# Kernel tuning notes

Measured on AMD Instinct MI355X. Metric: run time of the kernel, lower is better.

## Reference

```python
import jax, jax.numpy as jnp
import numpy as np

NUM_EXPERT = 8
TOP_K = 1


def setup_inputs() -> dict:
    key = jax.random.key(0)
    ks = jax.random.split(key, 6)
    B, S, D, E, F = 8, 2048, 768, 8, 469
    scale = 0.02
    return {
        "x": jax.random.normal(ks[0], (B, S, D), dtype=jnp.float32),
        "Wg": jax.random.normal(ks[1], (E, D), dtype=jnp.float32) * scale,
        "bg": jnp.zeros((E,), dtype=jnp.float32),
        "W1": jax.random.normal(ks[2], (E, F, D), dtype=jnp.float32) * scale,
        "W2": jax.random.normal(ks[3], (E, F, D), dtype=jnp.float32) * scale,
        "W3": jax.random.normal(ks[4], (E, D, F), dtype=jnp.float32) * scale,
    }


def reference(x, Wg, bg, W1, W2, W3):
    # x: [B, S, D]; Wg: [E, D]; W1/W2: [E, F, D] (torch Linear layout [out,in]); W3: [E, D, F]
    B, S, D = x.shape
    E = Wg.shape[0]
    xf = x.reshape(B * S, D)  # [T, D]

    # gating: top-k over expert logits, softmax over the selected logits
    gate = xf @ Wg.T + bg  # [T, E]
    vals, idx = jax.lax.top_k(gate, TOP_K)  # [T, K]
    probs = jax.nn.softmax(vals, axis=-1)  # [T, K] (all ones for K=1)

    # combine weights per (token, expert): sum over k slots of onehot * prob
    dispatch = jnp.sum(
        jax.nn.one_hot(idx, E, dtype=x.dtype) * probs[..., None], axis=1
    )  # [T, E]

    # dense grouped SwiGLU FFN over all experts, combined by dispatch weights
    h = jax.nn.silu(jnp.einsum("td,efd->tef", xf, W1)) * jnp.einsum(
        "td,efd->tef", xf, W2
    )  # [T, E, F]
    out = jnp.einsum("tef,edf,te->td", h, W3, dispatch)  # [T, D]
    return out.reshape(B, S, D)
```

## Files before the change

kernel.cpp:

```cpp
#include <hip/hip_runtime.h>
#include <hip/hip_bf16.h>
#include <stdint.h>

#define TT 16384
#define DD 768
#define EE 8
#define FF 469
#define FP 512
#define NCHUNK (TT / 64)
#define MAXTILES 136

typedef __attribute__((ext_vector_type(8))) short s16x8;
typedef __attribute__((ext_vector_type(4))) float f32x4;

__device__ __forceinline__ ushort f2bf(float f) {
  uint32_t u = __builtin_bit_cast(uint32_t, f);
  u += 0x7fffu + ((u >> 16) & 1u);
  return (ushort)(u >> 16);
}

__device__ __forceinline__ void gload16(const void* g, void* l) {
  __builtin_amdgcn_global_load_lds((const __attribute__((address_space(1))) unsigned int*)g,
                                   (__attribute__((address_space(3))) unsigned int*)l,
                                   16, 0, 0);
}

__global__ __launch_bounds__(256) void gate_conv_kernel(
    const float* __restrict__ x, const float* __restrict__ Wg,
    const float* __restrict__ bg, int* __restrict__ eidx,
    ushort* __restrict__ xbf) {
  __shared__ float4 wgs[EE * DD / 4];
  int tid = threadIdx.x;
  for (int i = tid; i < EE * DD / 4; i += 256) wgs[i] = ((const float4*)Wg)[i];
  __syncthreads();

  int t = blockIdx.x * 4 + (tid >> 6);
  int lane = tid & 63;
  const float4* xr = (const float4*)(x + (size_t)t * DD);
  float4 xv[3];
#pragma unroll
  for (int k = 0; k < 3; ++k) xv[k] = xr[lane + 64 * k];

  float acc[EE];
#pragma unroll
  for (int e = 0; e < EE; ++e) acc[e] = 0.f;
#pragma unroll
  for (int k = 0; k < 3; ++k) {
#pragma unroll
    for (int e = 0; e < EE; ++e) {
      float4 w = wgs[e * 192 + lane + 64 * k];
      acc[e] += xv[k].x * w.x + xv[k].y * w.y + xv[k].z * w.z + xv[k].w * w.w;
    }
  }

  uint2* xd = (uint2*)(xbf + (size_t)t * DD);
#pragma unroll
  for (int k = 0; k < 3; ++k) {
    union { ushort u[4]; uint2 w; } p;
    p.u[0] = f2bf(xv[k].x); p.u[1] = f2bf(xv[k].y);
    p.u[2] = f2bf(xv[k].z); p.u[3] = f2bf(xv[k].w);
    xd[lane + 64 * k] = p.w;
  }

#pragma unroll
  for (int off = 32; off; off >>= 1) {
#pragma unroll
    for (int e = 0; e < EE; ++e) acc[e] += __shfl_down(acc[e], off);
  }
  if (lane == 0) {
    float best = acc[0] + bg[0];
    int bi = 0;
#pragma unroll
    for (int e = 1; e < EE; ++e) {
      float v = acc[e] + bg[e];
      if (v > best) { best = v; bi = e; }
    }
    eidx[t] = bi;
  }
}

__global__ void hist_kernel(const int* __restrict__ eidx, int* __restrict__ cnt) {
  int c = blockIdx.x * 4 + (threadIdx.x >> 6);
  int lane = threadIdx.x & 63;
  int v = eidx[c * 64 + lane];
#pragma unroll
  for (int e = 0; e < EE; ++e) {
    unsigned long long me = __ballot(v == e);
    if (lane == 0) cnt[e * NCHUNK + c] = __popcll(me);
  }
}

__global__ void scan_kernel(const int* __restrict__ cnt, int* __restrict__ scanEx,
                            int* __restrict__ offs, int* __restrict__ tileE,
                            int* __restrict__ tileT0) {
  int e = threadIdx.x >> 6;
  int lane = threadIdx.x & 63;
  __shared__ int totals[EE];
  int carry = 0;
#pragma unroll
  for (int g = 0; g < NCHUNK / 64; ++g) {
    int v = cnt[e * NCHUNK + g * 64 + lane];
    int s = v;
#pragma unroll
    for (int d = 1; d < 64; d <<= 1) {
      int t = __shfl_up(s, d);
      if (lane >= d) s += t;
    }
    scanEx[e * NCHUNK + g * 64 + lane] = carry + s - v;
    carry += __shfl(s, 63);
  }
  if (lane == 0) totals[e] = carry;
  __syncthreads();
  if (threadIdx.x == 0) {
    int s = 0;
    for (int e2 = 0; e2 < EE; ++e2) { offs[e2] = s; s += totals[e2]; }
    offs[EE] = s;
    int idx = 0;
    for (int e2 = 0; e2 < EE; ++e2) {
      int nt = (totals[e2] + 127) >> 7;
      for (int j = 0; j < nt; ++j) { tileE[idx] = e2; tileT0[idx] = j << 7; ++idx; }
    }
    for (; idx < MAXTILES; ++idx) tileE[idx] = -1;
  }
}

__global__ void scatter2_kernel(const int* __restrict__ eidx, const int* __restrict__ offs,
                                const int* __restrict__ scanEx, int* __restrict__ perm) {
  int c = blockIdx.x * 4 + (threadIdx.x >> 6);
  int lane = threadIdx.x & 63;
  int t = c * 64 + lane;
  int v = eidx[t];
  unsigned long long mym = 0;
#pragma unroll
  for (int e = 0; e < EE; ++e) {
    unsigned long long me = __ballot(v == e);
    if (v == e) mym = me;
  }
  int rank = __popcll(mym & ((1ULL << lane) - 1ULL));
  perm[offs[v] + scanEx[v * NCHUNK + c] + rank] = t;
}

__global__ void convw12_kernel(const float* __restrict__ W1, const float* __restrict__ W2,
                               ushort* __restrict__ w12b) {
  const int n4 = EE * 2 * FP * (DD / 4);
  for (int i = blockIdx.x * blockDim.x + threadIdx.x; i < n4; i += gridDim.x * blockDim.x) {
    int d4 = i % (DD / 4);
    int er = i / (DD / 4);
    int row = er & 1023;
    int e = er >> 10;
    int f = row >> 1;
    union { ushort u[4]; uint2 w; } p;
    if (f < FF) {
      const float* src = ((row & 1) ? W2 : W1) + ((size_t)e * FF + f) * DD;
      float4 v = ((const float4*)src)[d4];
      p.u[0] = f2bf(v.x); p.u[1] = f2bf(v.y); p.u[2] = f2bf(v.z); p.u[3] = f2bf(v.w);
    } else {
      p.w.x = 0u; p.w.y = 0u;
    }
    ((uint2*)w12b)[i] = p.w;
  }
}

__global__ void convw3_kernel(const float* __restrict__ W3, ushort* __restrict__ w3b) {
  const int n = EE * DD * FP;
  for (int i = blockIdx.x * blockDim.x + threadIdx.x; i < n; i += gridDim.x * blockDim.x) {
    int f = i % FP;
    int ed = i / FP;
    float v = (f < FF) ? W3[(size_t)ed * FF + f] : 0.f;
    w3b[i] = f2bf(v);
  }
}

__global__ __launch_bounds__(256) void ffn1_kernel(
    const ushort* __restrict__ xbf, const ushort* __restrict__ w12b,
    const int* __restrict__ perm, const int* __restrict__ offs,
    const int* __restrict__ tileE, const int* __restrict__ tileT0,
    ushort* __restrict__ hbf) {
  int bid = blockIdx.x;
  int L = (bid & 7) * MAXTILES + (bid >> 3);
  int ti = L >> 3;
  int y = L & 7;
  int e = tileE[ti];
  if (e < 0) return;
  int tile0 = tileT0[ti];
  int gOff = offs[e];
  int Ne = offs[e + 1] - gOff;
  int n0 = y * 128;

  __shared__ __align__(16) short As[3][128 * 32];
  __shared__ __align__(16) short Bs[3][128 * 32];

  int tid = threadIdx.x;
  int w = tid >> 6, lane = tid & 63;
  int lr = lane >> 2, lg = lane & 3;

  int r0 = w * 32 + lr, r1 = r0 + 16;
  int g0 = lg ^ ((r0 >> 1) & 3);
  int g1 = lg ^ ((r1 >> 1) & 3);
  int last = gOff + Ne - 1;
  int tok0 = perm[min(gOff + tile0 + r0, last)];
  int tok1 = perm[min(gOff + tile0 + r1, last)];
  const ushort* asrc0 = xbf + (size_t)tok0 * DD + g0 * 8;
  const ushort* asrc1 = xbf + (size_t)tok1 * DD + g1 * 8;
  const ushort* bsrc0 = w12b + ((size_t)(e << 10) + n0 + r0) * DD + g0 * 8;
  const ushort* bsrc1 = w12b + ((size_t)(e << 10) + n0 + r1) * DD + g1 * 8;
  int sdst0 = (w * 32) * 32;
  int sdst1 = sdst0 + 16 * 32;

  int wr = w >> 1, wc = w & 1;
  int lrow = lane & 15, kh = lane >> 4;
  int aoff[4], boff[4];
#pragma unroll
  for (int m = 0; m < 4; ++m) {
    int ra = wr * 64 + m * 16 + lrow;
    aoff[m] = ra * 32 + (kh ^ ((ra >> 1) & 3)) * 8;
    int rb = wc * 64 + m * 16 + lrow;
    boff[m] = rb * 32 + (kh ^ ((rb >> 1) & 3)) * 8;
  }

  f32x4 acc[4][4];
  f32x4 zero = {0.f, 0.f, 0.f, 0.f};
#pragma unroll
  for (int m = 0; m < 4; ++m)
#pragma unroll
    for (int n = 0; n < 4; ++n) acc[m][n] = zero;

  gload16(asrc0, &As[0][sdst0]);
  gload16(asrc1, &As[0][sdst1]);
  gload16(bsrc0, &Bs[0][sdst0]);
  gload16(bsrc1, &Bs[0][sdst1]);
  gload16(asrc0 + 32, &As[1][sdst0]);
  gload16(asrc1 + 32, &As[1][sdst1]);
  gload16(bsrc0 + 32, &Bs[1][sdst0]);
  gload16(bsrc1 + 32, &Bs[1][sdst1]);

  const int NT = DD / 32;
#pragma unroll
  for (int t = 0; t < NT; ++t) {
    const int cur = t % 3;
    if (t < NT - 1) asm volatile("s_waitcnt vmcnt(4)" ::: "memory");
    else            asm volatile("s_waitcnt vmcnt(0)" ::: "memory");
    __builtin_amdgcn_s_barrier();
    __builtin_amdgcn_sched_barrier(0);
    if (t + 2 < NT) {
      const int nb = (t + 2) % 3;
      int k = (t + 2) * 32;
      gload16(asrc0 + k, &As[nb][sdst0]);
      gload16(asrc1 + k, &As[nb][sdst1]);
      gload16(bsrc0 + k, &Bs[nb][sdst0]);
      gload16(bsrc1 + k, &Bs[nb][sdst1]);
    }
    s16x8 af[4], bfr[4];
#pragma unroll
    for (int m = 0; m < 4; ++m) af[m] = *(const s16x8*)&As[cur][aoff[m]];
#pragma unroll
    for (int n = 0; n < 4; ++n) bfr[n] = *(const s16x8*)&Bs[cur][boff[n]];
    __builtin_amdgcn_s_setprio(1);
#pragma unroll
    for (int m = 0; m < 4; ++m)
#pragma unroll
      for (int n = 0; n < 4; ++n)
        acc[m][n] = __builtin_amdgcn_mfma_f32_16x16x32_bf16(af[m], bfr[n], acc[m][n], 0, 0, 0);
    __builtin_amdgcn_s_setprio(0);
  }

#pragma unroll
  for (int m = 0; m < 4; ++m) {
    int rbase = tile0 + wr * 64 + m * 16 + kh * 4;
#pragma unroll
    for (int n = 0; n < 4; ++n) {
      int f = (n0 + wc * 64 + n * 16 + lrow) >> 1;
#pragma unroll
      for (int r = 0; r < 4; ++r) {
        float val = acc[m][n][r];
        float par = __shfl_xor(val, 1);
        float u = (lane & 1) ? par : val;
        float vv = (lane & 1) ? val : par;
        float h = (u / (1.f + __expf(-u))) * vv;
        int gr = rbase + r;
        if (!(lane & 1) && gr < Ne)
          hbf[(size_t)(gOff + gr) * FP + f] = f2bf(h);
      }
    }
  }
}

__global__ __launch_bounds__(256) void ffn2_kernel(
    const ushort* __restrict__ hbf, const ushort* __restrict__ w3b,
    const int* __restrict__ perm, const int* __restrict__ offs,
    const int* __restrict__ tileE, const int* __restrict__ tileT0,
    float* __restrict__ out) {
  int bid = blockIdx.x;
  int L = (bid & 7) * 102 + (bid >> 3);
  int ti = L / 6;
  int y = L % 6;
  int e = tileE[ti];
  if (e < 0) return;
  int tile0 = tileT0[ti];
  int gOff = offs[e];
  int Ne = offs[e + 1] - gOff;
  int d0 = y * 128;

  __shared__ __align__(16) short As[3][128 * 32];
  __shared__ __align__(16) short Bs[3][128 * 32];

  int tid = threadIdx.x;
  int w = tid >> 6, lane = tid & 63;
  int lr = lane >> 2, lg = lane & 3;

  int r0 = w * 32 + lr, r1 = r0 + 16;
  int g0 = lg ^ ((r0 >> 1) & 3);
  int g1 = lg ^ ((r1 >> 1) & 3);
  int last = gOff + Ne - 1;
  const ushort* asrc0 = hbf + (size_t)min(gOff + tile0 + r0, last) * FP + g0 * 8;
  const ushort* asrc1 = hbf + (size_t)min(gOff + tile0 + r1, last) * FP + g1 * 8;
  const ushort* bsrc0 = w3b + ((size_t)e * DD + d0 + r0) * FP + g0 * 8;
  const ushort* bsrc1 = w3b + ((size_t)e * DD + d0 + r1) * FP + g1 * 8;
  int sdst0 = (w * 32) * 32;
  int sdst1 = sdst0 + 16 * 32;

  int wr = w >> 1, wc = w & 1;
  int lrow = lane & 15, kh = lane >> 4;
  int aoff[4], boff[4];
#pragma unroll
  for (int m = 0; m < 4; ++m) {
    int ra = wr * 64 + m * 16 + lrow;
    aoff[m] = ra * 32 + (kh ^ ((ra >> 1) & 3)) * 8;
    int rb = wc * 64 + m * 16 + lrow;
    boff[m] = rb * 32 + (kh ^ ((rb >> 1) & 3)) * 8;
  }

  f32x4 acc[4][4];
  f32x4 zero = {0.f, 0.f, 0.f, 0.f};
#pragma unroll
  for (int m = 0; m < 4; ++m)
#pragma unroll
    for (int n = 0; n < 4; ++n) acc[m][n] = zero;

  gload16(asrc0, &As[0][sdst0]);
  gload16(asrc1, &As[0][sdst1]);
  gload16(bsrc0, &Bs[0][sdst0]);
  gload16(bsrc1, &Bs[0][sdst1]);
  gload16(asrc0 + 32, &As[1][sdst0]);
  gload16(asrc1 + 32, &As[1][sdst1]);
  gload16(bsrc0 + 32, &Bs[1][sdst0]);
  gload16(bsrc1 + 32, &Bs[1][sdst1]);

  const int NT = FP / 32;
#pragma unroll
  for (int t = 0; t < NT; ++t) {
    const int cur = t % 3;
    if (t < NT - 1) asm volatile("s_waitcnt vmcnt(4)" ::: "memory");
    else            asm volatile("s_waitcnt vmcnt(0)" ::: "memory");
    __builtin_amdgcn_s_barrier();
    __builtin_amdgcn_sched_barrier(0);
    if (t + 2 < NT) {
      const int nb = (t + 2) % 3;
      int k = (t + 2) * 32;
      gload16(asrc0 + k, &As[nb][sdst0]);
      gload16(asrc1 + k, &As[nb][sdst1]);
      gload16(bsrc0 + k, &Bs[nb][sdst0]);
      gload16(bsrc1 + k, &Bs[nb][sdst1]);
    }
    s16x8 af[4], bfr[4];
#pragma unroll
    for (int m = 0; m < 4; ++m) af[m] = *(const s16x8*)&As[cur][aoff[m]];
#pragma unroll
    for (int n = 0; n < 4; ++n) bfr[n] = *(const s16x8*)&Bs[cur][boff[n]];
    __builtin_amdgcn_s_setprio(1);
#pragma unroll
    for (int m = 0; m < 4; ++m)
#pragma unroll
      for (int n = 0; n < 4; ++n)
        acc[m][n] = __builtin_amdgcn_mfma_f32_16x16x32_bf16(af[m], bfr[n], acc[m][n], 0, 0, 0);
    __builtin_amdgcn_s_setprio(0);
  }

#pragma unroll
  for (int m = 0; m < 4; ++m) {
#pragma unroll
    for (int r = 0; r < 4; ++r) {
      int gr = tile0 + wr * 64 + m * 16 + kh * 4 + r;
      if (gr < Ne) {
        int t = perm[gOff + gr];
        float* orow = out + (size_t)t * DD + d0 + wc * 64;
#pragma unroll
        for (int n = 0; n < 4; ++n) orow[n * 16 + lrow] = acc[m][n][r];
      }
    }
  }
}

extern "C" void kernel_launch(void* const* d_in, const int* in_sizes, int n_in,
                              void* d_out, int out_size, void* d_ws, size_t ws_size,
                              hipStream_t stream) {
  const float* x = (const float*)d_in[0];
  const float* Wg = (const float*)d_in[1];
  const float* bg = (const float*)d_in[2];
  const float* W1 = (const float*)d_in[3];
  const float* W2 = (const float*)d_in[4];
  const float* W3 = (const float*)d_in[5];
  float* out = (float*)d_out;

  char* ws = (char*)d_ws;
  int* eidx = (int*)ws;
  int* perm = (int*)(ws + 65536);
  int* offs = (int*)(ws + 131072);
  int* cnt = (int*)(ws + 131072 + 128);
  int* scanEx = (int*)(ws + 131072 + 128 + 8192);
  int* tileE = (int*)(ws + 131072 + 128 + 16384);
  int* tileT0 = tileE + MAXTILES + 8;
  ushort* xbf = (ushort*)(ws + 262144);
  ushort* w12b = xbf + (size_t)TT * DD;
  ushort* w3b = w12b + (size_t)EE * 2 * FP * DD;
  ushort* hbf = w3b + (size_t)EE * DD * FP;

  gate_conv_kernel<<<TT / 4, 256, 0, stream>>>(x, Wg, bg, eidx, xbf);
  convw12_kernel<<<2048, 256, 0, stream>>>(W1, W2, w12b);
  convw3_kernel<<<2048, 256, 0, stream>>>(W3, w3b);
  hist_kernel<<<NCHUNK / 4, 256, 0, stream>>>(eidx, cnt);
  scan_kernel<<<1, 512, 0, stream>>>(cnt, scanEx, offs, tileE, tileT0);
  scatter2_kernel<<<NCHUNK / 4, 256, 0, stream>>>(eidx, offs, scanEx, perm);
  ffn1_kernel<<<8 * MAXTILES, 256, 0, stream>>>(xbf, w12b, perm, offs, tileE, tileT0, hbf);
  ffn2_kernel<<<6 * MAXTILES, 256, 0, stream>>>(hbf, w3b, perm, offs, tileE, tileT0, out);
}
```

Before: 122.6 us.

## Load GEMM A-operand directly into registers and fuse histogram and weight conversions

Both grouped-GEMM kernels now skip staging the A operand (gathered x rows, or h rows) in LDS. Each lane loads its MFMA A fragments straight from global memory into registers, prefetching one k-step ahead, while B keeps the LDS triple buffer. The per-chunk expert histogram now uses atomics inside the gating kernel after a memset, which removes one kernel launch. The two weight-conversion kernels are merged into one, and W3 conversion writes four elements per thread. The direct global A loads are less coalesced and add register pressure, and the hand-tuned vmcnt count has to match the new mix of loads.

Result: slower. 165.6 us (+35.1%).

```diff
diff --git a/kernel.cpp b/kernel.cpp
--- a/kernel.cpp
+++ b/kernel.cpp
@@ -28,7 +28,7 @@
 __global__ __launch_bounds__(256) void gate_conv_kernel(
     const float* __restrict__ x, const float* __restrict__ Wg,
     const float* __restrict__ bg, int* __restrict__ eidx,
-    ushort* __restrict__ xbf) {
+    ushort* __restrict__ xbf, int* __restrict__ cnt) {
   __shared__ float4 wgs[EE * DD / 4];
   int tid = threadIdx.x;
   for (int i = tid; i < EE * DD / 4; i += 256) wgs[i] = ((const float4*)Wg)[i];
@@ -76,17 +76,7 @@
       if (v > best) { best = v; bi = e; }
     }
     eidx[t] = bi;
-  }
-}
-
-__global__ void hist_kernel(const int* __restrict__ eidx, int* __restrict__ cnt) {
-  int c = blockIdx.x * 4 + (threadIdx.x >> 6);
-  int lane = threadIdx.x & 63;
-  int v = eidx[c * 64 + lane];
-#pragma unroll
-  for (int e = 0; e < EE; ++e) {
-    unsigned long long me = __ballot(v == e);
-    if (lane == 0) cnt[e * NCHUNK + c] = __popcll(me);
+    atomicAdd(&cnt[bi * NCHUNK + (t >> 6)], 1);
   }
 }
 
@@ -140,34 +130,40 @@
   perm[offs[v] + scanEx[v * NCHUNK + c] + rank] = t;
 }
 
-__global__ void convw12_kernel(const float* __restrict__ W1, const float* __restrict__ W2,
-                               ushort* __restrict__ w12b) {
-  const int n4 = EE * 2 * FP * (DD / 4);
-  for (int i = blockIdx.x * blockDim.x + threadIdx.x; i < n4; i += gridDim.x * blockDim.x) {
-    int d4 = i % (DD / 4);
-    int er = i / (DD / 4);
-    int row = er & 1023;
-    int e = er >> 10;
-    int f = row >> 1;
-    union { ushort u[4]; uint2 w; } p;
-    if (f < FF) {
-      const float* src = ((row & 1) ? W2 : W1) + ((size_t)e * FF + f) * DD;
-      float4 v = ((const float4*)src)[d4];
-      p.u[0] = f2bf(v.x); p.u[1] = f2bf(v.y); p.u[2] = f2bf(v.z); p.u[3] = f2bf(v.w);
+#define N12 (EE * 2 * FP * (DD / 4))
+#define N3  (EE * DD * (FP / 4))
+__global__ void convw_kernel(const float* __restrict__ W1, const float* __restrict__ W2,
+                             const float* __restrict__ W3, ushort* __restrict__ w12b,
+                             ushort* __restrict__ w3b) {
+  for (int i = blockIdx.x * blockDim.x + threadIdx.x; i < N12 + N3;
+       i += gridDim.x * blockDim.x) {
+    if (i < N12) {
+      int d4 = i % (DD / 4);
+      int er = i / (DD / 4);
+      int row = er & 1023;
+      int e = er >> 10;
+      int f = row >> 1;
+      union { ushort u[4]; uint2 w; } p;
+      if (f < FF) {
+        const float* src = ((row & 1) ? W2 : W1) + ((size_t)e * FF + f) * DD;
+        float4 v = ((const float4*)src)[d4];
+        p.u[0] = f2bf(v.x); p.u[1] = f2bf(v.y); p.u[2] = f2bf(v.z); p.u[3] = f2bf(v.w);
+      } else {
+        p.w.x = 0u; p.w.y = 0u;
+      }
+      ((uint2*)w12b)[i] = p.w;
     } else {
-      p.w.x = 0u; p.w.y = 0u;
-    }
-    ((uint2*)w12b)[i] = p.w;
-  }
-}
-
-__global__ void convw3_kernel(const float* __restrict__ W3, ushort* __restrict__ w3b) {
-  const int n = EE * DD * FP;
-  for (int i = blockIdx.x * blockDim.x + threadIdx.x; i < n; i += gridDim.x * blockDim.x) {
-    int f = i % FP;
-    int ed = i / FP;
-    float v = (f < FF) ? W3[(size_t)ed * FF + f] : 0.f;
-    w3b[i] = f2bf(v);
+      int j = i - N12;
+      int f4 = (j % (FP / 4)) * 4;
+      int ed = j / (FP / 4);
+      union { ushort u[4]; uint2 w; } p;
+#pragma unroll
+      for (int q = 0; q < 4; ++q) {
+        int f = f4 + q;
+        p.u[q] = (f < FF) ? f2bf(W3[(size_t)ed * FF + f]) : (ushort)0;
+      }
+      ((uint2*)w3b)[(size_t)ed * (FP / 4) + (f4 >> 2)] = p.w;
+    }
   }
 }
 
@@ -187,7 +183,6 @@
   int Ne = offs[e + 1] - gOff;
   int n0 = y * 128;
 
-  __shared__ __align__(16) short As[3][128 * 32];
   __shared__ __align__(16) short Bs[3][128 * 32];
 
   int tid = threadIdx.x;
@@ -197,11 +192,6 @@
   int r0 = w * 32 + lr, r1 = r0 + 16;
   int g0 = lg ^ ((r0 >> 1) & 3);
   int g1 = lg ^ ((r1 >> 1) & 3);
-  int last = gOff + Ne - 1;
-  int tok0 = perm[min(gOff + tile0 + r0, last)];
-  int tok1 = perm[min(gOff + tile0 + r1, last)];
-  const ushort* asrc0 = xbf + (size_t)tok0 * DD + g0 * 8;
-  const ushort* asrc1 = xbf + (size_t)tok1 * DD + g1 * 8;
   const ushort* bsrc0 = w12b + ((size_t)(e << 10) + n0 + r0) * DD + g0 * 8;
   const ushort* bsrc1 = w12b + ((size_t)(e << 10) + n0 + r1) * DD + g1 * 8;
   int sdst0 = (w * 32) * 32;
@@ -209,13 +199,20 @@
 
   int wr = w >> 1, wc = w & 1;
   int lrow = lane & 15, kh = lane >> 4;
-  int aoff[4], boff[4];
+  int boff[4];
+#pragma unroll
+  for (int n = 0; n < 4; ++n) {
+    int rb = wc * 64 + n * 16 + lrow;
+    boff[n] = rb * 32 + (kh ^ ((rb >> 1) & 3)) * 8;
+  }
+
+  int last = gOff + Ne - 1;
+  const ushort* aptr[4];
 #pragma unroll
   for (int m = 0; m < 4; ++m) {
     int ra = wr * 64 + m * 16 + lrow;
-    aoff[m] = ra * 32 + (kh ^ ((ra >> 1) & 3)) * 8;
-    int rb = wc * 64 + m * 16 + lrow;
-    boff[m] = rb * 32 + (kh ^ ((rb >> 1) & 3)) * 8;
+    int tok = perm[min(gOff + tile0 + ra, last)];
+    aptr[m] = xbf + (size_t)tok * DD + kh * 8;
   }
 
   f32x4 acc[4][4];
@@ -225,34 +222,32 @@
 #pragma unroll
     for (int n = 0; n < 4; ++n) acc[m][n] = zero;
 
-  gload16(asrc0, &As[0][sdst0]);
-  gload16(asrc1, &As[0][sdst1]);
   gload16(bsrc0, &Bs[0][sdst0]);
   gload16(bsrc1, &Bs[0][sdst1]);
-  gload16(asrc0 + 32, &As[1][sdst0]);
-  gload16(asrc1 + 32, &As[1][sdst1]);
   gload16(bsrc0 + 32, &Bs[1][sdst0]);
   gload16(bsrc1 + 32, &Bs[1][sdst1]);
+  s16x8 aC[4], aN[4];
+#pragma unroll
+  for (int m = 0; m < 4; ++m) aC[m] = *(const s16x8*)aptr[m];
 
   const int NT = DD / 32;
 #pragma unroll
   for (int t = 0; t < NT; ++t) {
     const int cur = t % 3;
-    if (t < NT - 1) asm volatile("s_waitcnt vmcnt(4)" ::: "memory");
-    else            asm volatile("s_waitcnt vmcnt(0)" ::: "memory");
+    asm volatile("s_waitcnt vmcnt(6)" ::: "memory");
     __builtin_amdgcn_s_barrier();
     __builtin_amdgcn_sched_barrier(0);
     if (t + 2 < NT) {
-      const int nb = (t + 2) % 3;
       int k = (t + 2) * 32;
-      gload16(asrc0 + k, &As[nb][sdst0]);
-      gload16(asrc1 + k, &As[nb][sdst1]);
-      gload16(bsrc0 + k, &Bs[nb][sdst0]);
-      gload16(bsrc1 + k, &Bs[nb][sdst1]);
-    }
-    s16x8 af[4], bfr[4];
-#pragma unroll
-    for (int m = 0; m < 4; ++m) af[m] = *(const s16x8*)&As[cur][aoff[m]];
+      gload16(bsrc0 + k, &Bs[(t + 2) % 3][sdst0]);
+      gload16(bsrc1 + k, &Bs[(t + 2) % 3][sdst1]);
+    }
+    if (t + 1 < NT) {
+      int k = (t + 1) * 32;
+#pragma unroll
+      for (int m = 0; m < 4; ++m) aN[m] = *(const s16x8*)(aptr[m] + k);
+    }
+    s16x8 bfr[4];
 #pragma unroll
     for (int n = 0; n < 4; ++n) bfr[n] = *(const s16x8*)&Bs[cur][boff[n]];
     __builtin_amdgcn_s_setprio(1);
@@ -260,8 +255,10 @@
     for (int m = 0; m < 4; ++m)
 #pragma unroll
       for (int n = 0; n < 4; ++n)
-        acc[m][n] = __builtin_amdgcn_mfma_f32_16x16x32_bf16(af[m], bfr[n], acc[m][n], 0, 0, 0);
+        acc[m][n] = __builtin_amdgcn_mfma_f32_16x16x32_bf16(aC[m], bfr[n], acc[m][n], 0, 0, 0);
     __builtin_amdgcn_s_setprio(0);
+#pragma unroll
+    for (int m = 0; m < 4; ++m) aC[m] = aN[m];
   }
 
 #pragma unroll
@@ -301,7 +298,6 @@
   int Ne = offs[e + 1] - gOff;
   int d0 = y * 128;
 
-  __shared__ __align__(16) short As[3][128 * 32];
   __shared__ __align__(16) short Bs[3][128 * 32];
 
   int tid = threadIdx.x;
@@ -311,9 +307,6 @@
   int r0 = w * 32 + lr, r1 = r0 + 16;
   int g0 = lg ^ ((r0 >> 1) & 3);
   int g1 = lg ^ ((r1 >> 1) & 3);
-  int last = gOff + Ne - 1;
-  const ushort* asrc0 = hbf + (size_t)min(gOff + tile0 + r0, last) * FP + g0 * 8;
-  const ushort* asrc1 = hbf + (size_t)min(gOff + tile0 + r1, last) * FP + g1 * 8;
   const ushort* bsrc0 = w3b + ((size_t)e * DD + d0 + r0) * FP + g0 * 8;
   const ushort* bsrc1 = w3b + ((size_t)e * DD + d0 + r1) * FP + g1 * 8;
   int sdst0 = (w * 32) * 32;
@@ -321,13 +314,19 @@
 
   int wr = w >> 1, wc = w & 1;
   int lrow = lane & 15, kh = lane >> 4;
-  int aoff[4], boff[4];
+  int boff[4];
+#pragma unroll
+  for (int n = 0; n < 4; ++n) {
+    int rb = wc * 64 + n * 16 + lrow;
+    boff[n] = rb * 32 + (kh ^ ((rb >> 1) & 3)) * 8;
+  }
+
+  int last = gOff + Ne - 1;
+  const ushort* aptr[4];
 #pragma unroll
   for (int m = 0; m < 4; ++m) {
     int ra = wr * 64 + m * 16 + lrow;
-    aoff[m] = ra * 32 + (kh ^ ((ra >> 1) & 3)) * 8;
-    int rb = wc * 64 + m * 16 + lrow;
-    boff[m] = rb * 32 + (kh ^ ((rb >> 1) & 3)) * 8;
+    aptr[m] = hbf + (size_t)min(gOff + tile0 + ra, last) * FP + kh * 8;
   }
 
   f32x4 acc[4][4];
@@ -337,34 +336,32 @@
 #pragma unroll
     for (int n = 0; n < 4; ++n) acc[m][n] = zero;
 
-  gload16(asrc0, &As[0][sdst0]);
-  gload16(asrc1, &As[0][sdst1]);
   gload16(bsrc0, &Bs[0][sdst0]);
   gload16(bsrc1, &Bs[0][sdst1]);
-  gload16(asrc0 + 32, &As[1][sdst0]);
-  gload16(asrc1 + 32, &As[1][sdst1]);
   gload16(bsrc0 + 32, &Bs[1][sdst0]);
   gload16(bsrc1 + 32, &Bs[1][sdst1]);
+  s16x8 aC[4], aN[4];
+#pragma unroll
+  for (int m = 0; m < 4; ++m) aC[m] = *(const s16x8*)aptr[m];
 
   const int NT = FP / 32;
 #pragma unroll
   for (int t = 0; t < NT; ++t) {
     const int cur = t % 3;
-    if (t < NT - 1) asm volatile("s_waitcnt vmcnt(4)" ::: "memory");
-    else            asm volatile("s_waitcnt vmcnt(0)" ::: "memory");
+    asm volatile("s_waitcnt vmcnt(6)" ::: "memory");
     __builtin_amdgcn_s_barrier();
     __builtin_amdgcn_sched_barrier(0);
     if (t + 2 < NT) {
-      const int nb = (t + 2) % 3;
       int k = (t + 2) * 32;
-      gload16(asrc0 + k, &As[nb][sdst0]);
-      gload16(asrc1 + k, &As[nb][sdst1]);
-      gload16(bsrc0 + k, &Bs[nb][sdst0]);
-      gload16(bsrc1 + k, &Bs[nb][sdst1]);
-    }
-    s16x8 af[4], bfr[4];
-#pragma unroll
-    for (int m = 0; m < 4; ++m) af[m] = *(const s16x8*)&As[cur][aoff[m]];
+      gload16(bsrc0 + k, &Bs[(t + 2) % 3][sdst0]);
+      gload16(bsrc1 + k, &Bs[(t + 2) % 3][sdst1]);
+    }
+    if (t + 1 < NT) {
+      int k = (t + 1) * 32;
+#pragma unroll
+      for (int m = 0; m < 4; ++m) aN[m] = *(const s16x8*)(aptr[m] + k);
+    }
+    s16x8 bfr[4];
 #pragma unroll
     for (int n = 0; n < 4; ++n) bfr[n] = *(const s16x8*)&Bs[cur][boff[n]];
     __builtin_amdgcn_s_setprio(1);
@@ -372,8 +369,10 @@
     for (int m = 0; m < 4; ++m)
 #pragma unroll
       for (int n = 0; n < 4; ++n)
-        acc[m][n] = __builtin_amdgcn_mfma_f32_16x16x32_bf16(af[m], bfr[n], acc[m][n], 0, 0, 0);
+        acc[m][n] = __builtin_amdgcn_mfma_f32_16x16x32_bf16(aC[m], bfr[n], acc[m][n], 0, 0, 0);
     __builtin_amdgcn_s_setprio(0);
+#pragma unroll
+    for (int m = 0; m < 4; ++m) aC[m] = aN[m];
   }
 
 #pragma unroll
@@ -415,12 +414,11 @@
   ushort* w3b = w12b + (size_t)EE * 2 * FP * DD;
   ushort* hbf = w3b + (size_t)EE * DD * FP;
 
-  gate_conv_kernel<<<TT / 4, 256, 0, stream>>>(x, Wg, bg, eidx, xbf);
-  convw12_kernel<<<2048, 256, 0, stream>>>(W1, W2, w12b);
-  convw3_kernel<<<2048, 256, 0, stream>>>(W3, w3b);
-  hist_kernel<<<NCHUNK / 4, 256, 0, stream>>>(eidx, cnt);
+  hipMemsetAsync(cnt, 0, EE * NCHUNK * 4, stream);
+  gate_conv_kernel<<<TT / 4, 256, 0, stream>>>(x, Wg, bg, eidx, xbf, cnt);
+  convw_kernel<<<2048, 256, 0, stream>>>(W1, W2, W3, w12b, w3b);
   scan_kernel<<<1, 512, 0, stream>>>(cnt, scanEx, offs, tileE, tileT0);
   scatter2_kernel<<<NCHUNK / 4, 256, 0, stream>>>(eidx, offs, scanEx, perm);
   ffn1_kernel<<<8 * MAXTILES, 256, 0, stream>>>(xbf, w12b, perm, offs, tileE, tileT0, hbf);
-  ffn2_kernel<<<6 * MAXTILES, 256, 0, stream>>>(hbf, w3b, perm, offs, tileE, tileT0, out);
-}
+  ffn2_kernel<<<8 * 102, 256, 0, stream>>>(hbf, w3b, perm, offs, tileE, tileT0, out);
+}
```

## Fuse gate, histogram and weight conversion; run two tiles per GEMM block

Applied to the files above, without the earlier changes.

Merges the gating/bf16-conversion, histogram (now done with atomics into a memset buffer) and the W1/W2/W3 conversion kernels into one launch. The W3 conversion is vectorised to four elements per thread. The ffn1 and ffn2 grids are halved so each block processes two consecutive tiles in sequence. This cuts launch count and per-block setup, but serialises tile work within a block, which may lower parallelism and load balance on the GEMMs.

Result: slower. 125.5 us (+2.3%).

```diff
diff --git a/kernel.cpp b/kernel.cpp
--- a/kernel.cpp
+++ b/kernel.cpp
@@ -25,68 +25,95 @@
                                    16, 0, 0);
 }
 
-__global__ __launch_bounds__(256) void gate_conv_kernel(
+#define N12 (EE * 2 * FP * (DD / 4))
+#define N3  (EE * DD * (FP / 4))
+__global__ __launch_bounds__(256) void prep_kernel(
     const float* __restrict__ x, const float* __restrict__ Wg,
-    const float* __restrict__ bg, int* __restrict__ eidx,
-    ushort* __restrict__ xbf) {
-  __shared__ float4 wgs[EE * DD / 4];
+    const float* __restrict__ bg, const float* __restrict__ W1,
+    const float* __restrict__ W2, const float* __restrict__ W3,
+    int* __restrict__ eidx, ushort* __restrict__ xbf, int* __restrict__ cnt,
+    ushort* __restrict__ w12b, ushort* __restrict__ w3b) {
   int tid = threadIdx.x;
-  for (int i = tid; i < EE * DD / 4; i += 256) wgs[i] = ((const float4*)Wg)[i];
-  __syncthreads();
-
-  int t = blockIdx.x * 4 + (tid >> 6);
-  int lane = tid & 63;
-  const float4* xr = (const float4*)(x + (size_t)t * DD);
-  float4 xv[3];
-#pragma unroll
-  for (int k = 0; k < 3; ++k) xv[k] = xr[lane + 64 * k];
-
-  float acc[EE];
-#pragma unroll
-  for (int e = 0; e < EE; ++e) acc[e] = 0.f;
-#pragma unroll
-  for (int k = 0; k < 3; ++k) {
-#pragma unroll
-    for (int e = 0; e < EE; ++e) {
-      float4 w = wgs[e * 192 + lane + 64 * k];
-      acc[e] += xv[k].x * w.x + xv[k].y * w.y + xv[k].z * w.z + xv[k].w * w.w;
-    }
-  }
-
-  uint2* xd = (uint2*)(xbf + (size_t)t * DD);
-#pragma unroll
-  for (int k = 0; k < 3; ++k) {
-    union { ushort u[4]; uint2 w; } p;
-    p.u[0] = f2bf(xv[k].x); p.u[1] = f2bf(xv[k].y);
-    p.u[2] = f2bf(xv[k].z); p.u[3] = f2bf(xv[k].w);
-    xd[lane + 64 * k] = p.w;
-  }
-
-#pragma unroll
-  for (int off = 32; off; off >>= 1) {
-#pragma unroll
-    for (int e = 0; e < EE; ++e) acc[e] += __shfl_down(acc[e], off);
-  }
-  if (lane == 0) {
-    float best = acc[0] + bg[0];
-    int bi = 0;
-#pragma unroll
-    for (int e = 1; e < EE; ++e) {
-      float v = acc[e] + bg[e];
-      if (v > best) { best = v; bi = e; }
-    }
-    eidx[t] = bi;
-  }
-}
-
-__global__ void hist_kernel(const int* __restrict__ eidx, int* __restrict__ cnt) {
-  int c = blockIdx.x * 4 + (threadIdx.x >> 6);
-  int lane = threadIdx.x & 63;
-  int v = eidx[c * 64 + lane];
-#pragma unroll
-  for (int e = 0; e < EE; ++e) {
-    unsigned long long me = __ballot(v == e);
-    if (lane == 0) cnt[e * NCHUNK + c] = __popcll(me);
+  if (blockIdx.x < TT / 4) {
+    __shared__ float4 wgs[EE * DD / 4];
+    for (int i = tid; i < EE * DD / 4; i += 256) wgs[i] = ((const float4*)Wg)[i];
+    __syncthreads();
+
+    int t = blockIdx.x * 4 + (tid >> 6);
+    int lane = tid & 63;
+    const float4* xr = (const float4*)(x + (size_t)t * DD);
+    float4 xv[3];
+#pragma unroll
+    for (int k = 0; k < 3; ++k) xv[k] = xr[lane + 64 * k];
+
+    float acc[EE];
+#pragma unroll
+    for (int e = 0; e < EE; ++e) acc[e] = 0.f;
+#pragma unroll
+    for (int k = 0; k < 3; ++k) {
+#pragma unroll
+      for (int e = 0; e < EE; ++e) {
+        float4 w = wgs[e * 192 + lane + 64 * k];
+        acc[e] += xv[k].x * w.x + xv[k].y * w.y + xv[k].z * w.z + xv[k].w * w.w;
+      }
+    }
+
+    uint2* xd = (uint2*)(xbf + (size_t)t * DD);
+#pragma unroll
+    for (int k = 0; k < 3; ++k) {
+      union { ushort u[4]; uint2 w; } p;
+      p.u[0] = f2bf(xv[k].x); p.u[1] = f2bf(xv[k].y);
+      p.u[2] = f2bf(xv[k].z); p.u[3] = f2bf(xv[k].w);
+      xd[lane + 64 * k] = p.w;
+    }
+
+#pragma unroll
+    for (int off = 32; off; off >>= 1) {
+#pragma unroll
+      for (int e = 0; e < EE; ++e) acc[e] += __shfl_down(acc[e], off);
+    }
+    if (lane == 0) {
+      float best = acc[0] + bg[0];
+      int bi = 0;
+#pragma unroll
+      for (int e = 1; e < EE; ++e) {
+        float v = acc[e] + bg[e];
+        if (v > best) { best = v; bi = e; }
+      }
+      eidx[t] = bi;
+      atomicAdd(&cnt[bi * NCHUNK + (t >> 6)], 1);
+    }
+  } else {
+    int vb = blockIdx.x - TT / 4;
+    for (int i = vb * 256 + tid; i < N12 + N3; i += 2048 * 256) {
+      if (i < N12) {
+        int d4 = i % (DD / 4);
+        int er = i / (DD / 4);
+        int row = er & 1023;
+        int e = er >> 10;
+        int f = row >> 1;
+        union { ushort u[4]; uint2 w; } p;
+        if (f < FF) {
+          const float* src = ((row & 1) ? W2 : W1) + ((size_t)e * FF + f) * DD;
+          float4 v = ((const float4*)src)[d4];
+          p.u[0] = f2bf(v.x); p.u[1] = f2bf(v.y); p.u[2] = f2bf(v.z); p.u[3] = f2bf(v.w);
+        } else {
+          p.w.x = 0u; p.w.y = 0u;
+        }
+        ((uint2*)w12b)[i] = p.w;
+      } else {
+        int j = i - N12;
+        int f4 = (j % (FP / 4)) * 4;
+        int ed = j / (FP / 4);
+        union { ushort u[4]; uint2 w; } p;
+#pragma unroll
+        for (int q = 0; q < 4; ++q) {
+          int f = f4 + q;
+          p.u[q] = (f < FF) ? f2bf(W3[(size_t)ed * FF + f]) : (ushort)0;
+        }
+        ((uint2*)w3b)[(size_t)ed * (FP / 4) + (f4 >> 2)] = p.w;
+      }
+    }
   }
 }
 
@@ -140,52 +167,13 @@
   perm[offs[v] + scanEx[v * NCHUNK + c] + rank] = t;
 }
 
-__global__ void convw12_kernel(const float* __restrict__ W1, const float* __restrict__ W2,
-                               ushort* __restrict__ w12b) {
-  const int n4 = EE * 2 * FP * (DD / 4);
-  for (int i = blockIdx.x * blockDim.x + threadIdx.x; i < n4; i += gridDim.x * blockDim.x) {
-    int d4 = i % (DD / 4);
-    int er = i / (DD / 4);
-    int row = er & 1023;
-    int e = er >> 10;
-    int f = row >> 1;
-    union { ushort u[4]; uint2 w; } p;
-    if (f < FF) {
-      const float* src = ((row & 1) ? W2 : W1) + ((size_t)e * FF + f) * DD;
-      float4 v = ((const float4*)src)[d4];
-      p.u[0] = f2bf(v.x); p.u[1] = f2bf(v.y); p.u[2] = f2bf(v.z); p.u[3] = f2bf(v.w);
-    } else {
-      p.w.x = 0u; p.w.y = 0u;
-    }
-    ((uint2*)w12b)[i] = p.w;
-  }
-}
-
-__global__ void convw3_kernel(const float* __restrict__ W3, ushort* __restrict__ w3b) {
-  const int n = EE * DD * FP;
-  for (int i = blockIdx.x * blockDim.x + threadIdx.x; i < n; i += gridDim.x * blockDim.x) {
-    int f = i % FP;
-    int ed = i / FP;
-    float v = (f < FF) ? W3[(size_t)ed * FF + f] : 0.f;
-    w3b[i] = f2bf(v);
-  }
-}
-
 __global__ __launch_bounds__(256) void ffn1_kernel(
     const ushort* __restrict__ xbf, const ushort* __restrict__ w12b,
     const int* __restrict__ perm, const int* __restrict__ offs,
     const int* __restrict__ tileE, const int* __restrict__ tileT0,
     ushort* __restrict__ hbf) {
   int bid = blockIdx.x;
-  int L = (bid & 7) * MAXTILES + (bid >> 3);
-  int ti = L >> 3;
-  int y = L & 7;
-  int e = tileE[ti];
-  if (e < 0) return;
-  int tile0 = tileT0[ti];
-  int gOff = offs[e];
-  int Ne = offs[e + 1] - gOff;
-  int n0 = y * 128;
+  int Lbase = (bid & 7) * 68 + (bid >> 3);
 
   __shared__ __align__(16) short As[3][128 * 32];
   __shared__ __align__(16) short Bs[3][128 * 32];
@@ -193,93 +181,108 @@
   int tid = threadIdx.x;
   int w = tid >> 6, lane = tid & 63;
   int lr = lane >> 2, lg = lane & 3;
-
-  int r0 = w * 32 + lr, r1 = r0 + 16;
-  int g0 = lg ^ ((r0 >> 1) & 3);
-  int g1 = lg ^ ((r1 >> 1) & 3);
-  int last = gOff + Ne - 1;
-  int tok0 = perm[min(gOff + tile0 + r0, last)];
-  int tok1 = perm[min(gOff + tile0 + r1, last)];
-  const ushort* asrc0 = xbf + (size_t)tok0 * DD + g0 * 8;
-  const ushort* asrc1 = xbf + (size_t)tok1 * DD + g1 * 8;
-  const ushort* bsrc0 = w12b + ((size_t)(e << 10) + n0 + r0) * DD + g0 * 8;
-  const ushort* bsrc1 = w12b + ((size_t)(e << 10) + n0 + r1) * DD + g1 * 8;
+  int wr = w >> 1, wc = w & 1;
+  int lrow = lane & 15, kh = lane >> 4;
+
   int sdst0 = (w * 32) * 32;
   int sdst1 = sdst0 + 16 * 32;
 
-  int wr = w >> 1, wc = w & 1;
-  int lrow = lane & 15, kh = lane >> 4;
-  int aoff[4], boff[4];
-#pragma unroll
-  for (int m = 0; m < 4; ++m) {
-    int ra = wr * 64 + m * 16 + lrow;
-    aoff[m] = ra * 32 + (kh ^ ((ra >> 1) & 3)) * 8;
-    int rb = wc * 64 + m * 16 + lrow;
-    boff[m] = rb * 32 + (kh ^ ((rb >> 1) & 3)) * 8;
-  }
-
-  f32x4 acc[4][4];
-  f32x4 zero = {0.f, 0.f, 0.f, 0.f};
-#pragma unroll
-  for (int m = 0; m < 4; ++m)
-#pragma unroll
-    for (int n = 0; n < 4; ++n) acc[m][n] = zero;
-
-  gload16(asrc0, &As[0][sdst0]);
-  gload16(asrc1, &As[0][sdst1]);
-  gload16(bsrc0, &Bs[0][sdst0]);
-  gload16(bsrc1, &Bs[0][sdst1]);
-  gload16(asrc0 + 32, &As[1][sdst0]);
-  gload16(asrc1 + 32, &As[1][sdst1]);
-  gload16(bsrc0 + 32, &Bs[1][sdst0]);
-  gload16(bsrc1 + 32, &Bs[1][sdst1]);
-
-  const int NT = DD / 32;
-#pragma unroll
-  for (int t = 0; t < NT; ++t) {
-    const int cur = t % 3;
-    if (t < NT - 1) asm volatile("s_waitcnt vmcnt(4)" ::: "memory");
-    else            asm volatile("s_waitcnt vmcnt(0)" ::: "memory");
+#pragma unroll
+  for (int pass = 0; pass < 2; ++pass) {
+    int L = Lbase * 2 + pass;
+    int ti = L >> 3;
+    int y = L & 7;
+    int e = tileE[ti];
+    if (e < 0) continue;
+    int tile0 = tileT0[ti];
+    int gOff = offs[e];
+    int Ne = offs[e + 1] - gOff;
+    int n0 = y * 128;
+
+    int r0 = w * 32 + lr, r1 = r0 + 16;
+    int g0 = lg ^ ((r0 >> 1) & 3);
+    int g1 = lg ^ ((r1 >> 1) & 3);
+    int last = gOff + Ne - 1;
+    int tok0 = perm[min(gOff + tile0 + r0, last)];
+    int tok1 = perm[min(gOff + tile0 + r1, last)];
+    const ushort* asrc0 = xbf + (size_t)tok0 * DD + g0 * 8;
+    const ushort* asrc1 = xbf + (size_t)tok1 * DD + g1 * 8;
+    const ushort* bsrc0 = w12b + ((size_t)(e << 10) + n0 + r0) * DD + g0 * 8;
+    const ushort* bsrc1 = w12b + ((size_t)(e << 10) + n0 + r1) * DD + g1 * 8;
+
+    int aoff[4], boff[4];
+#pragma unroll
+    for (int m = 0; m < 4; ++m) {
+      int ra = wr * 64 + m * 16 + lrow;
+      aoff[m] = ra * 32 + (kh ^ ((ra >> 1) & 3)) * 8;
+      int rb = wc * 64 + m * 16 + lrow;
+      boff[m] = rb * 32 + (kh ^ ((rb >> 1) & 3)) * 8;
+    }
+
+    f32x4 acc[4][4];
+    f32x4 zero = {0.f, 0.f, 0.f, 0.f};
+#pragma unroll
+    for (int m = 0; m < 4; ++m)
+#pragma unroll
+      for (int n = 0; n < 4; ++n) acc[m][n] = zero;
+
     __builtin_amdgcn_s_barrier();
-    __builtin_amdgcn_sched_barrier(0);
-    if (t + 2 < NT) {
-      const int nb = (t + 2) % 3;
-      int k = (t + 2) * 32;
-      gload16(asrc0 + k, &As[nb][sdst0]);
-      gload16(asrc1 + k, &As[nb][sdst1]);
-      gload16(bsrc0 + k, &Bs[nb][sdst0]);
-      gload16(bsrc1 + k, &Bs[nb][sdst1]);
-    }
-    s16x8 af[4], bfr[4];
-#pragma unroll
-    for (int m = 0; m < 4; ++m) af[m] = *(const s16x8*)&As[cur][aoff[m]];
-#pragma unroll
-    for (int n = 0; n < 4; ++n) bfr[n] = *(const s16x8*)&Bs[cur][boff[n]];
-    __builtin_amdgcn_s_setprio(1);
-#pragma unroll
-    for (int m = 0; m < 4; ++m)
-#pragma unroll
-      for (int n = 0; n < 4; ++n)
-        acc[m][n] = __builtin_amdgcn_mfma_f32_16x16x32_bf16(af[m], bfr[n], acc[m][n], 0, 0, 0);
-    __builtin_amdgcn_s_setprio(0);
-  }
-
-#pragma unroll
-  for (int m = 0; m < 4; ++m) {
-    int rbase = tile0 + wr * 64 + m * 16 + kh * 4;
-#pragma unroll
-    for (int n = 0; n < 4; ++n) {
-      int f = (n0 + wc * 64 + n * 16 + lrow) >> 1;
-#pragma unroll
-      for (int r = 0; r < 4; ++r) {
-        float val = acc[m][n][r];
-        float par = __shfl_xor(val, 1);
-        float u = (lane & 1) ? par : val;
-        float vv = (lane & 1) ? val : par;
-        float h = (u / (1.f + __expf(-u))) * vv;
-        int gr = rbase + r;
-        if (!(lane & 1) && gr < Ne)
-          hbf[(size_t)(gOff + gr) * FP + f] = f2bf(h);
+    gload16(asrc0, &As[0][sdst0]);
+    gload16(asrc1, &As[0][sdst1]);
+    gload16(bsrc0, &Bs[0][sdst0]);
+    gload16(bsrc1, &Bs[0][sdst1]);
+    gload16(asrc0 + 32, &As[1][sdst0]);
+    gload16(asrc1 + 32, &As[1][sdst1]);
+    gload16(bsrc0 + 32, &Bs[1][sdst0]);
+    gload16(bsrc1 + 32, &Bs[1][sdst1]);
+
+    const int NT = DD / 32;
+#pragma unroll
+    for (int t = 0; t < NT; ++t) {
+      const int cur = t % 3;
+      if (t < NT - 1) asm volatile("s_waitcnt vmcnt(4)" ::: "memory");
+      else            asm volatile("s_waitcnt vmcnt(0)" ::: "memory");
+      __builtin_amdgcn_s_barrier();
+      __builtin_amdgcn_sched_barrier(0);
+      if (t + 2 < NT) {
+        const int nb = (t + 2) % 3;
+        int k = (t + 2) * 32;
+        gload16(asrc0 + k, &As[nb][sdst0]);
+        gload16(asrc1 + k, &As[nb][sdst1]);
+        gload16(bsrc0 + k, &Bs[nb][sdst0]);
+        gload16(bsrc1 + k, &Bs[nb][sdst1]);
+      }
+      s16x8 af[4], bfr[4];
+#pragma unroll
+      for (int m = 0; m < 4; ++m) af[m] = *(const s16x8*)&As[cur][aoff[m]];
+#pragma unroll
+      for (int n = 0; n < 4; ++n) bfr[n] = *(const s16x8*)&Bs[cur][boff[n]];
+      __builtin_amdgcn_s_setprio(1);
+#pragma unroll
+      for (int m = 0; m < 4; ++m)
+#pragma unroll
+        for (int n = 0; n < 4; ++n)
+          acc[m][n] = __builtin_amdgcn_mfma_f32_16x16x32_bf16(af[m], bfr[n], acc[m][n], 0, 0, 0);
+      __builtin_amdgcn_s_setprio(0);
+    }
+
+#pragma unroll
+    for (int m = 0; m < 4; ++m) {
+      int rbase = tile0 + wr * 64 + m * 16 + kh * 4;
+#pragma unroll
+      for (int n = 0; n < 4; ++n) {
+        int f = (n0 + wc * 64 + n * 16 + lrow) >> 1;
+#pragma unroll
+        for (int r = 0; r < 4; ++r) {
+          float val = acc[m][n][r];
+          float par = __shfl_xor(val, 1);
+          float u = (lane & 1) ? par : val;
+          float vv = (lane & 1) ? val : par;
+          float h = (u / (1.f + __expf(-u))) * vv;
+          int gr = rbase + r;
+          if (!(lane & 1) && gr < Ne)
+            hbf[(size_t)(gOff + gr) * FP + f] = f2bf(h);
+        }
       }
     }
   }
@@ -291,15 +294,7 @@
     const int* __restrict__ tileE, const int* __restrict__ tileT0,
     float* __restrict__ out) {
   int bid = blockIdx.x;
-  int L = (bid & 7) * 102 + (bid >> 3);
-  int ti = L / 6;
-  int y = L % 6;
-  int e = tileE[ti];
-  if (e < 0) return;
-  int tile0 = tileT0[ti];
-  int gOff = offs[e];
-  int Ne = offs[e + 1] - gOff;
-  int d0 = y * 128;
+  int Lbase = (bid & 7) * 51 + (bid >> 3);
 
   __shared__ __align__(16) short As[3][128 * 32];
   __shared__ __align__(16) short Bs[3][128 * 32];
@@ -307,85 +302,100 @@
   int tid = threadIdx.x;
   int w = tid >> 6, lane = tid & 63;
   int lr = lane >> 2, lg = lane & 3;
-
-  int r0 = w * 32 + lr, r1 = r0 + 16;
-  int g0 = lg ^ ((r0 >> 1) & 3);
-  int g1 = lg ^ ((r1 >> 1) & 3);
-  int last = gOff + Ne - 1;
-  const ushort* asrc0 = hbf + (size_t)min(gOff + tile0 + r0, last) * FP + g0 * 8;
-  const ushort* asrc1 = hbf + (size_t)min(gOff + tile0 + r1, last) * FP + g1 * 8;
-  const ushort* bsrc0 = w3b + ((size_t)e * DD + d0 + r0) * FP + g0 * 8;
-  const ushort* bsrc1 = w3b + ((size_t)e * DD + d0 + r1) * FP + g1 * 8;
+  int wr = w >> 1, wc = w & 1;
+  int lrow = lane & 15, kh = lane >> 4;
+
   int sdst0 = (w * 32) * 32;
   int sdst1 = sdst0 + 16 * 32;
 
-  int wr = w >> 1, wc = w & 1;
-  int lrow = lane & 15, kh = lane >> 4;
-  int aoff[4], boff[4];
-#pragma unroll
-  for (int m = 0; m < 4; ++m) {
-    int ra = wr * 64 + m * 16 + lrow;
-    aoff[m] = ra * 32 + (kh ^ ((ra >> 1) & 3)) * 8;
-    int rb = wc * 64 + m * 16 + lrow;
-    boff[m] = rb * 32 + (kh ^ ((rb >> 1) & 3)) * 8;
-  }
-
-  f32x4 acc[4][4];
-  f32x4 zero = {0.f, 0.f, 0.f, 0.f};
-#pragma unroll
-  for (int m = 0; m < 4; ++m)
-#pragma unroll
-    for (int n = 0; n < 4; ++n) acc[m][n] = zero;
-
-  gload16(asrc0, &As[0][sdst0]);
-  gload16(asrc1, &As[0][sdst1]);
-  gload16(bsrc0, &Bs[0][sdst0]);
-  gload16(bsrc1, &Bs[0][sdst1]);
-  gload16(asrc0 + 32, &As[1][sdst0]);
-  gload16(asrc1 + 32, &As[1][sdst1]);
-  gload16(bsrc0 + 32, &Bs[1][sdst0]);
-  gload16(bsrc1 + 32, &Bs[1][sdst1]);
-
-  const int NT = FP / 32;
-#pragma unroll
-  for (int t = 0; t < NT; ++t) {
-    const int cur = t % 3;
-    if (t < NT - 1) asm volatile("s_waitcnt vmcnt(4)" ::: "memory");
-    else            asm volatile("s_waitcnt vmcnt(0)" ::: "memory");
+#pragma unroll
+  for (int pass = 0; pass < 2; ++pass) {
+    int L = Lbase * 2 + pass;
+    int ti = L / 6;
+    int y = L % 6;
+    int e = tileE[ti];
+    if (e < 0) continue;
+    int tile0 = tileT0[ti];
+    int gOff = offs[e];
+    int Ne = offs[e + 1] - gOff;
+    int d0 = y * 128;
+
+    int r0 = w * 32 + lr, r1 = r0 + 16;
+    int g0 = lg ^ ((r0 >> 1) & 3);
+    int g1 = lg ^ ((r1 >> 1) & 3);
+    int last = gOff + Ne - 1;
+    const ushort* asrc0 = hbf + (size_t)min(gOff + tile0 + r0, last) * FP + g0 * 8;
+    const ushort* asrc1 = hbf + (size_t)min(gOff + tile0 + r1, last) * FP + g1 * 8;
+    const ushort* bsrc0 = w3b + ((size_t)e * DD + d0 + r0) * FP + g0 * 8;
+    const ushort* bsrc1 = w3b + ((size_t)e * DD + d0 + r1) * FP + g1 * 8;
+
+    int aoff[4], boff[4];
+#pragma unroll
+    for (int m = 0; m < 4; ++m) {
+      int ra = wr * 64 + m * 16 + lrow;
+      aoff[m] = ra * 32 + (kh ^ ((ra >> 1) & 3)) * 8;
+      int rb = wc * 64 + m * 16 + lrow;
+      boff[m] = rb * 32 + (kh ^ ((rb >> 1) & 3)) * 8;
+    }
+
+    f32x4 acc[4][4];
+    f32x4 zero = {0.f, 0.f, 0.f, 0.f};
+#pragma unroll
+    for (int m = 0; m < 4; ++m)
+#pragma unroll
+      for (int n = 0; n < 4; ++n) acc[m][n] = zero;
+
     __builtin_amdgcn_s_barrier();
-    __builtin_amdgcn_sched_barrier(0);
-    if (t + 2 < NT) {
-      const int nb = (t + 2) % 3;
-      int k = (t + 2) * 32;
-      gload16(asrc0 + k, &As[nb][sdst0]);
-      gload16(asrc1 + k, &As[nb][sdst1]);
-      gload16(bsrc0 + k, &Bs[nb][sdst0]);
-      gload16(bsrc1 + k, &Bs[nb][sdst1]);
-    }
-    s16x8 af[4], bfr[4];
-#pragma unroll
-    for (int m = 0; m < 4; ++m) af[m] = *(const s16x8*)&As[cur][aoff[m]];
-#pragma unroll
-    for (int n = 0; n < 4; ++n) bfr[n] = *(const s16x8*)&Bs[cur][boff[n]];
-    __builtin_amdgcn_s_setprio(1);
-#pragma unroll
-    for (int m = 0; m < 4; ++m)
-#pragma unroll
-      for (int n = 0; n < 4; ++n)
-        acc[m][n] = __builtin_amdgcn_mfma_f32_16x16x32_bf16(af[m], bfr[n], acc[m][n], 0, 0, 0);
-    __builtin_amdgcn_s_setprio(0);
-  }
-
-#pragma unroll
-  for (int m = 0; m < 4; ++m) {
-#pragma unroll
-    for (int r = 0; r < 4; ++r) {
-      int gr = tile0 + wr * 64 + m * 16 + kh * 4 + r;
-      if (gr < Ne) {
-        int t = perm[gOff + gr];
-        float* orow = out + (size_t)t * DD + d0 + wc * 64;
-#pragma unroll
-        for (int n = 0; n < 4; ++n) orow[n * 16 + lrow] = acc[m][n][r];
+    gload16(asrc0, &As[0][sdst0]);
+    gload16(asrc1, &As[0][sdst1]);
+    gload16(bsrc0, &Bs[0][sdst0]);
+    gload16(bsrc1, &Bs[0][sdst1]);
+    gload16(asrc0 + 32, &As[1][sdst0]);
+    gload16(asrc1 + 32, &As[1][sdst1]);
+    gload16(bsrc0 + 32, &Bs[1][sdst0]);
+    gload16(bsrc1 + 32, &Bs[1][sdst1]);
+
+    const int NT = FP / 32;
+#pragma unroll
+    for (int t = 0; t < NT; ++t) {
+      const int cur = t % 3;
+      if (t < NT - 1) asm volatile("s_waitcnt vmcnt(4)" ::: "memory");
+      else            asm volatile("s_waitcnt vmcnt(0)" ::: "memory");
+      __builtin_amdgcn_s_barrier();
+      __builtin_amdgcn_sched_barrier(0);
+      if (t + 2 < NT) {
+        const int nb = (t + 2) % 3;
+        int k = (t + 2) * 32;
+        gload16(asrc0 + k, &As[nb][sdst0]);
+        gload16(asrc1 + k, &As[nb][sdst1]);
+        gload16(bsrc0 + k, &Bs[nb][sdst0]);
+        gload16(bsrc1 + k, &Bs[nb][sdst1]);
+      }
+      s16x8 af[4], bfr[4];
+#pragma unroll
+      for (int m = 0; m < 4; ++m) af[m] = *(const s16x8*)&As[cur][aoff[m]];
+#pragma unroll
+      for (int n = 0; n < 4; ++n) bfr[n] = *(const s16x8*)&Bs[cur][boff[n]];
+      __builtin_amdgcn_s_setprio(1);
+#pragma unroll
+      for (int m = 0; m < 4; ++m)
+#pragma unroll
+        for (int n = 0; n < 4; ++n)
+          acc[m][n] = __builtin_amdgcn_mfma_f32_16x16x32_bf16(af[m], bfr[n], acc[m][n], 0, 0, 0);
+      __builtin_amdgcn_s_setprio(0);
+    }
+
+#pragma unroll
+    for (int m = 0; m < 4; ++m) {
+#pragma unroll
+      for (int r = 0; r < 4; ++r) {
+        int gr = tile0 + wr * 64 + m * 16 + kh * 4 + r;
+        if (gr < Ne) {
+          int t = perm[gOff + gr];
+          float* orow = out + (size_t)t * DD + d0 + wc * 64;
+#pragma unroll
+          for (int n = 0; n < 4; ++n) orow[n * 16 + lrow] = acc[m][n][r];
+        }
       }
     }
   }
@@ -415,12 +425,11 @@
   ushort* w3b = w12b + (size_t)EE * 2 * FP * DD;
   ushort* hbf = w3b + (size_t)EE * DD * FP;
 
-  gate_conv_kernel<<<TT / 4, 256, 0, stream>>>(x, Wg, bg, eidx, xbf);
-  convw12_kernel<<<2048, 256, 0, stream>>>(W1, W2, w12b);
-  convw3_kernel<<<2048, 256, 0, stream>>>(W3, w3b);
-  hist_kernel<<<NCHUNK / 4, 256, 0, stream>>>(eidx, cnt);
+  hipMemsetAsync(cnt, 0, EE * NCHUNK * 4, stream);
+  prep_kernel<<<TT / 4 + 2048, 256, 0, stream>>>(x, Wg, bg, W1, W2, W3,
+                                                 eidx, xbf, cnt, w12b, w3b);
   scan_kernel<<<1, 512, 0, stream>>>(cnt, scanEx, offs, tileE, tileT0);
   scatter2_kernel<<<NCHUNK / 4, 256, 0, stream>>>(eidx, offs, scanEx, perm);
-  ffn1_kernel<<<8 * MAXTILES, 256, 0, stream>>>(xbf, w12b, perm, offs, tileE, tileT0, hbf);
-  ffn2_kernel<<<6 * MAXTILES, 256, 0, stream>>>(hbf, w3b, perm, offs, tileE, tileT0, out);
-}
+  ffn1_kernel<<<544, 256, 0, stream>>>(xbf, w12b, perm, offs, tileE, tileT0, hbf);
+  ffn2_kernel<<<408, 256, 0, stream>>>(hbf, w3b, perm, offs, tileE, tileT0, out);
+}
```
